# Kernel tuning notes

Hardware: AMD Instinct MI355X
Metric: run time of the kernel (lower is better)

The kernel has to match this reference:

```python
import jax, jax.numpy as jnp
import numpy as np

NEG = -1e10  # matches the -10000000000.0 boundary padding in the torch code


def nw_forward(theta, A):
    """Needleman-Wunsch forward DP with softmax (logsumexp) operator.

    theta: (B, N, M) match potentials; A: (B,) gap penalty.
    Returns Vt: (B,) terminal alignment scores.
    Recursion: V[i,j] = theta[i-1,j-1] + logsumexp(A+V[i-1,j], V[i-1,j-1], A+V[i,j-1]).
    Implemented as scan over rows (i) with an inner scan over columns (j),
    which honors the sequential DP dependencies without Python loops.
    """
    B, N, M = theta.shape
    dtype = theta.dtype
    # V[0, :] row: V[0,0]=0, V[0,j]=NEG for j>=1
    row0 = jnp.full((B, M + 1), NEG, dtype).at[:, 0].set(0.0)

    def row_step(prev_row, th_row):
        # prev_row: (B, M+1) = V[i-1, 0..M]; th_row: (B, M) = theta[:, i-1, :]
        v_up = prev_row[:, 1:]     # V[i-1, j],   j = 1..M
        v_diag = prev_row[:, :-1]  # V[i-1, j-1], j = 1..M

        def col_step(v_left, inp):
            th_j, vu, vd = inp  # each (B,)
            # order (x, m, y) = (A+up, diag, A+left), matching torch stack(v1,v2,v3)
            v = jnp.stack([A + vu, vd, A + v_left], axis=-1)  # (B, 3)
            v_new = th_j + jax.nn.logsumexp(v, axis=-1)
            return v_new, v_new

        xs = (th_row.T, v_up.T, v_diag.T)  # leading axis M
        v_init = jnp.full((B,), NEG, dtype)  # V[i, 0]
        _, row_vals = jax.lax.scan(col_step, v_init, xs)  # (M, B)
        new_row = jnp.concatenate(
            [jnp.full((B, 1), NEG, dtype), row_vals.T], axis=1)  # (B, M+1)
        return new_row, None

    last_row, _ = jax.lax.scan(row_step, row0, jnp.moveaxis(theta, 1, 0))
    return last_row[:, M]  # Vt = V[:, N, M]


def setup_inputs() -> dict:
    key = jax.random.key(0)
    k1, k2 = jax.random.split(key)
    B, N, M = 32, 512, 512
    theta = jax.random.normal(k1, (B, N, M), dtype=jnp.float32)
    A = jax.random.normal(k2, (B,), dtype=jnp.float32)
    return {"theta": theta, "A": A}


def reference(theta, A):
    return nw_forward(theta, A)
```

## Files before the change

### kernel.cpp

```cpp
#include <hip/hip_runtime.h>
#include <math.h>

#define NEGV  -10000000000.0f
#define LOG2E 1.44269504088896340736f
#define LN2F  0.69314718055994530942f

typedef float f4 __attribute__((ext_vector_type(4)));

constexpr int CS    = 16;
constexpr int ROWS  = 80;
constexpr int WL    = 17;
constexpr int CHW   = ROWS * WL;
constexpr int KCMAX = 64;

__global__ __launch_bounds__(512, 2) void nw_kernel(
    const float* __restrict__ theta, const float* __restrict__ A,
    float* __restrict__ out, int N, int M)
{
    __shared__ float thS[8 * 2 * CHW];
    __shared__ float bndD[9 * KCMAX * 16];
    __shared__ int   flg[9 * KCMAX];

    const int tid = threadIdx.x;
    const int w   = tid >> 6;
    const int l   = tid & 63;
    const int j   = tid;
    const int b   = blockIdx.x;
    const int NW  = blockDim.x >> 6;

    for (int i = tid; i < 9 * KCMAX; i += blockDim.x) flg[i] = 0;
    __syncthreads();

    const float a2 = A[b] * LOG2E;
    const float* __restrict__ thb = theta + (size_t)b * N * M;
    const int NM = N * M;

    const int T  = N + M - 1;
    const int KC = (T + CS - 1) / CS;
    const int wstart = 64 * w;
    const int wend   = 64 * w + 63 + N - 1;
    const int ca = wstart / CS;
    const int cb = min(KC - 1, wend / CS);

    const int srow = l >> 4;
    const int sq   = l & 15;
    const int lanebase = srow * (M - 1) + 64 * w + 63 + sq;
    const int wrbase0 = (w * 2 + 0) * CHW + srow * WL + sq;
    const int wrbase1 = (w * 2 + 1) * CHW + srow * WL + sq;
    const int rdbase0 = (w * 2 + 0) * CHW + (63 - l) * WL;
    const int rdbase1 = (w * 2 + 1) * CHW + (63 - l) * WL;

    auto stage_load = [&](int cn, float* stg) {
        const int rb = CS * cn - 64 * w - 63;
        if (rb >= 0 && rb + (ROWS - 1) <= N - 1) {
            const float* p = thb + (size_t)rb * M;
            #pragma unroll
            for (int it = 0; it < 20; ++it) { stg[it] = p[lanebase]; p += 4 * (M - 1); }
        } else {
            const int rbM = rb * M;
            #pragma unroll
            for (int it = 0; it < 20; ++it) {
                int off = rbM + lanebase + it * 4 * (M - 1);
                off = min(max(off, 0), NM - 1);
                stg[it] = thb[off];
            }
        }
    };
    auto stage_write = [&](int cn, const float* stg) {
        const int wb = (cn & 1) ? wrbase1 : wrbase0;
        #pragma unroll
        for (int it = 0; it < 20; ++it) thS[wb + it * 4 * WL] = stg[it] * LOG2E;
    };
    auto wait_flag = [&](int idx) {
        if (__atomic_load_n(&flg[idx], __ATOMIC_ACQUIRE) == 0) {
            do { __builtin_amdgcn_s_sleep(1); }
            while (__atomic_load_n(&flg[idx], __ATOMIC_ACQUIRE) == 0);
        }
    };

    float v_prev = NEGV;
    float v_diag = (j == 0) ? 0.0f : NEGV;
    float bcarry = NEGV;

    {
        float s0[20];
        stage_load(ca, s0);
        stage_write(ca, s0);
        __asm__ volatile("s_waitcnt lgkmcnt(0)" ::: "memory");
    }
    if (w > 0) {
        wait_flag(w * KCMAX + (ca - 1));
        bcarry = bndD[(w * KCMAX + ca - 1) * 16 + 15];
    }

    float stg[20];
    bool have = (ca + 1 <= cb);
    if (have) stage_load(ca + 1, stg);

    for (int c = ca; c <= cb; ++c) {
        const int rdb = (c & 1) ? rdbase1 : rdbase0;
        float th[16];
        #pragma unroll
        for (int k = 0; k < 16; ++k) th[k] = thS[rdb + k * (WL + 1)];

        const bool need_bv = (w > 0) && (CS * c <= 64 * w + N - 1);
        float bv[16];
        if (need_bv) {
            wait_flag(w * KCMAX + c);
            const f4* src = (const f4*)&bndD[(w * KCMAX + c) * 16];
            f4 q0 = src[0], q1 = src[1], q2 = src[2], q3 = src[3];
            bv[0]=q0.x; bv[1]=q0.y; bv[2]=q0.z; bv[3]=q0.w;
            bv[4]=q1.x; bv[5]=q1.y; bv[6]=q1.z; bv[7]=q1.w;
            bv[8]=q2.x; bv[9]=q2.y; bv[10]=q2.z; bv[11]=q2.w;
            bv[12]=q3.x; bv[13]=q3.y; bv[14]=q3.z; bv[15]=q3.w;
        } else {
            #pragma unroll
            for (int k = 0; k < 16; ++k) bv[k] = NEGV;
        }

        float res[16];
        const bool full = (CS * c >= 64 * w + 63) &&
                          (CS * c + CS - 1 <= 64 * w + N - 1);
        if (full) {
            #pragma unroll
            for (int k = 0; k < 16; ++k) {
                float bk = (k == 0) ? bcarry : bv[k - 1];
                float vl = __int_as_float(__builtin_amdgcn_update_dpp(
                    __float_as_int(bk), __float_as_int(v_prev),
                    0x138 , 0xF, 0xF, false));
                float x = a2 + v_prev;
                float z = a2 + vl;
                float m = fmaxf(fmaxf(x, v_diag), z);
                float s = __builtin_amdgcn_exp2f(x - m)
                        + __builtin_amdgcn_exp2f(v_diag - m)
                        + __builtin_amdgcn_exp2f(z - m);
                float v = th[k] + m + __builtin_amdgcn_logf(s);
                res[k] = v;
                v_diag = vl;
                v_prev = v;
            }
        } else {
            const int tmj = CS * c - j;
            #pragma unroll
            for (int k = 0; k < 16; ++k) {
                float bk = (k == 0) ? bcarry : bv[k - 1];
                float vl = __int_as_float(__builtin_amdgcn_update_dpp(
                    __float_as_int(bk), __float_as_int(v_prev),
                    0x138, 0xF, 0xF, false));
                float x = a2 + v_prev;
                float z = a2 + vl;
                float m = fmaxf(fmaxf(x, v_diag), z);
                float s = __builtin_amdgcn_exp2f(x - m)
                        + __builtin_amdgcn_exp2f(v_diag - m)
                        + __builtin_amdgcn_exp2f(z - m);
                float v = th[k] + m + __builtin_amdgcn_logf(s);
                int dt = tmj + k;
                float vn = ((unsigned)dt < (unsigned)N) ? v
                                                        : (dt < 0 ? NEGV : v_prev);
                res[k] = vn;
                v_diag = vl;
                v_prev = vn;
            }
        }

        if (w < NW - 1 && l == 63) {
            f4* dst = (f4*)&bndD[((w + 1) * KCMAX + c) * 16];
            dst[0] = (f4){res[0],  res[1],  res[2],  res[3]};
            dst[1] = (f4){res[4],  res[5],  res[6],  res[7]};
            dst[2] = (f4){res[8],  res[9],  res[10], res[11]};
            dst[3] = (f4){res[12], res[13], res[14], res[15]};
            __atomic_store_n(&flg[(w + 1) * KCMAX + c], 1, __ATOMIC_RELEASE);
        }
        bcarry = bv[15];

        if (have) stage_write(c + 1, stg);
        have = (c + 2 <= cb);
        if (have) stage_load(c + 2, stg);
        __asm__ volatile("s_waitcnt lgkmcnt(0)" ::: "memory");
    }

    if (j == M - 1) out[b] = v_prev * LN2F;
}

extern "C" void kernel_launch(void* const* d_in, const int* in_sizes, int n_in,
                              void* d_out, int out_size, void* d_ws, size_t ws_size,
                              hipStream_t stream) {
    const float* theta = (const float*)d_in[0];
    const float* A     = (const float*)d_in[1];
    float* out = (float*)d_out;

    const int B  = in_sizes[1];
    const int NM = in_sizes[0] / B;
    int N = 1;
    while (N * N < NM) N <<= 1;
    const int M = NM / N;

    hipLaunchKernelGGL(nw_kernel, dim3(B), dim3(M), 0, stream,
                       theta, A, out, N, M);
}
```

Baseline: 182.2 us.

## Split each batch DP across two workgroups linked by global-memory boundary handoff

Each batch element now runs on two 256-thread workgroups, each holding four waves, instead of one 512-thread workgroup. The boundary column between the halves travels through the workspace in global memory, guarded by a magic-value flag, and the next chunk's boundary and flag are prefetched. The goal is to give each wave its own SIMD and reduce contention on the serial wavefront chain. The cost is cross-CU handoff latency, and the design depends on both workgroups being resident at once. The flags are never cleared between calls, so a later launch could read stale values. Local waits also drop the s_sleep backoff.

```diff
diff --git a/kernel.cpp b/kernel.cpp
--- a/kernel.cpp
+++ b/kernel.cpp
@@ -1,9 +1,10 @@
 #include <hip/hip_runtime.h>
 #include <math.h>
 
-#define NEGV  -10000000000.0f
-#define LOG2E 1.44269504088896340736f
-#define LN2F  0.69314718055994530942f
+#define NEGV   -10000000000.0f
+#define LOG2E  1.44269504088896340736f
+#define LN2F   0.69314718055994530942f
+#define MAGICF 0x5CA1AB1Eu
 
 typedef float f4 __attribute__((ext_vector_type(4)));
 
@@ -13,22 +14,24 @@
 constexpr int CHW   = ROWS * WL;
 constexpr int KCMAX = 64;
 
-__global__ __launch_bounds__(512, 2) void nw_kernel(
+__global__ __launch_bounds__(256, 1) void nw_kernel(
     const float* __restrict__ theta, const float* __restrict__ A,
-    float* __restrict__ out, int N, int M)
+    float* __restrict__ out, unsigned* __restrict__ gbnd,
+    unsigned* __restrict__ gflg, int N, int M)
 {
-    __shared__ float thS[8 * 2 * CHW];
-    __shared__ float bndD[9 * KCMAX * 16];
-    __shared__ int   flg[9 * KCMAX];
+    __shared__ float thS[4 * 2 * CHW];
+    __shared__ float bndL[4 * KCMAX * 16];
+    __shared__ int   flgL[4 * KCMAX];
 
     const int tid = threadIdx.x;
-    const int w   = tid >> 6;
+    const int wl  = tid >> 6;
     const int l   = tid & 63;
-    const int j   = tid;
-    const int b   = blockIdx.x;
-    const int NW  = blockDim.x >> 6;
-
-    for (int i = tid; i < 9 * KCMAX; i += blockDim.x) flg[i] = 0;
+    const int h   = blockIdx.x & 1;
+    const int b   = blockIdx.x >> 1;
+    const int wg  = 4 * h + wl;
+    const int j   = 64 * wg + l;
+
+    for (int i = tid; i < 4 * KCMAX; i += blockDim.x) flgL[i] = 0;
     __syncthreads();
 
     const float a2 = A[b] * LOG2E;
@@ -37,21 +40,24 @@
 
     const int T  = N + M - 1;
     const int KC = (T + CS - 1) / CS;
-    const int wstart = 64 * w;
-    const int wend   = 64 * w + 63 + N - 1;
-    const int ca = wstart / CS;
+    const int wend = 64 * wg + 63 + N - 1;
+    const int ca = (64 * wg) / CS;
     const int cb = min(KC - 1, wend / CS);
 
-    const int srow = l >> 4;
-    const int sq   = l & 15;
-    const int lanebase = srow * (M - 1) + 64 * w + 63 + sq;
-    const int wrbase0 = (w * 2 + 0) * CHW + srow * WL + sq;
-    const int wrbase1 = (w * 2 + 1) * CHW + srow * WL + sq;
-    const int rdbase0 = (w * 2 + 0) * CHW + (63 - l) * WL;
-    const int rdbase1 = (w * 2 + 1) * CHW + (63 - l) * WL;
+    const int srow = l >> 4, sq = l & 15;
+    const int lanebase = srow * (M - 1) + 64 * wg + 63 + sq;
+    const int wrbase0 = (wl * 2 + 0) * CHW + srow * WL + sq;
+    const int wrbase1 = (wl * 2 + 1) * CHW + srow * WL + sq;
+    const int rdbase0 = (wl * 2 + 0) * CHW + (63 - l) * WL;
+    const int rdbase1 = (wl * 2 + 1) * CHW + (63 - l) * WL;
+
+    unsigned* gB = gbnd + (size_t)b * KCMAX * 16;
+    unsigned* gF = gflg + b * KCMAX;
+    const bool gsrc = (h == 1) && (wl == 0);
+    const bool gpub = (h == 0) && (wl == 3);
 
     auto stage_load = [&](int cn, float* stg) {
-        const int rb = CS * cn - 64 * w - 63;
+        const int rb = CS * cn - 64 * wg - 63;
         if (rb >= 0 && rb + (ROWS - 1) <= N - 1) {
             const float* p = thb + (size_t)rb * M;
             #pragma unroll
@@ -71,12 +77,6 @@
         #pragma unroll
         for (int it = 0; it < 20; ++it) thS[wb + it * 4 * WL] = stg[it] * LOG2E;
     };
-    auto wait_flag = [&](int idx) {
-        if (__atomic_load_n(&flg[idx], __ATOMIC_ACQUIRE) == 0) {
-            do { __builtin_amdgcn_s_sleep(1); }
-            while (__atomic_load_n(&flg[idx], __ATOMIC_ACQUIRE) == 0);
-        }
-    };
 
     float v_prev = NEGV;
     float v_diag = (j == 0) ? 0.0f : NEGV;
@@ -88,14 +88,25 @@
         stage_write(ca, s0);
         __asm__ volatile("s_waitcnt lgkmcnt(0)" ::: "memory");
     }
-    if (w > 0) {
-        wait_flag(w * KCMAX + (ca - 1));
-        bcarry = bndD[(w * KCMAX + ca - 1) * 16 + 15];
+    if (wl > 0) {
+        const int idx = wl * KCMAX + (ca - 1);
+        while (__atomic_load_n(&flgL[idx], __ATOMIC_ACQUIRE) == 0) {}
+        bcarry = bndL[idx * 16 + 15];
+    } else if (gsrc) {
+        while (__hip_atomic_load(&gF[ca - 1], __ATOMIC_RELAXED,
+                                 __HIP_MEMORY_SCOPE_AGENT) != MAGICF)
+            __builtin_amdgcn_s_sleep(1);
+        bcarry = __uint_as_float(__hip_atomic_load(&gB[(ca - 1) * 16 + 15],
+                    __ATOMIC_RELAXED, __HIP_MEMORY_SCOPE_AGENT));
     }
 
     float stg[20];
     bool have = (ca + 1 <= cb);
     if (have) stage_load(ca + 1, stg);
+
+    unsigned gd[16];
+    unsigned fnext = 0;
+    bool gd_ok = false, fnext_valid = false;
 
     for (int c = ca; c <= cb; ++c) {
         const int rdb = (c & 1) ? rdbase1 : rdbase0;
@@ -103,24 +114,51 @@
         #pragma unroll
         for (int k = 0; k < 16; ++k) th[k] = thS[rdb + k * (WL + 1)];
 
-        const bool need_bv = (w > 0) && (CS * c <= 64 * w + N - 1);
+        const bool need_bv = (wg > 0) && (CS * c <= 64 * wg + N - 1);
         float bv[16];
         if (need_bv) {
-            wait_flag(w * KCMAX + c);
-            const f4* src = (const f4*)&bndD[(w * KCMAX + c) * 16];
-            f4 q0 = src[0], q1 = src[1], q2 = src[2], q3 = src[3];
-            bv[0]=q0.x; bv[1]=q0.y; bv[2]=q0.z; bv[3]=q0.w;
-            bv[4]=q1.x; bv[5]=q1.y; bv[6]=q1.z; bv[7]=q1.w;
-            bv[8]=q2.x; bv[9]=q2.y; bv[10]=q2.z; bv[11]=q2.w;
-            bv[12]=q3.x; bv[13]=q3.y; bv[14]=q3.z; bv[15]=q3.w;
+            if (!gsrc) {
+                const int idx = wl * KCMAX + c;
+                while (__atomic_load_n(&flgL[idx], __ATOMIC_ACQUIRE) == 0) {}
+                const f4* src = (const f4*)&bndL[idx * 16];
+                f4 q0 = src[0], q1 = src[1], q2 = src[2], q3 = src[3];
+                bv[0]=q0.x; bv[1]=q0.y; bv[2]=q0.z; bv[3]=q0.w;
+                bv[4]=q1.x; bv[5]=q1.y; bv[6]=q1.z; bv[7]=q1.w;
+                bv[8]=q2.x; bv[9]=q2.y; bv[10]=q2.z; bv[11]=q2.w;
+                bv[12]=q3.x; bv[13]=q3.y; bv[14]=q3.z; bv[15]=q3.w;
+            } else {
+                if (!gd_ok) {
+                    while (__hip_atomic_load(&gF[c], __ATOMIC_RELAXED,
+                                             __HIP_MEMORY_SCOPE_AGENT) != MAGICF)
+                        __builtin_amdgcn_s_sleep(1);
+                    #pragma unroll
+                    for (int k = 0; k < 16; ++k)
+                        gd[k] = __hip_atomic_load(&gB[c * 16 + k],
+                                    __ATOMIC_RELAXED, __HIP_MEMORY_SCOPE_AGENT);
+                }
+                #pragma unroll
+                for (int k = 0; k < 16; ++k) bv[k] = __uint_as_float(gd[k]);
+                gd_ok = false;
+                if (fnext_valid && fnext == MAGICF) {
+                    #pragma unroll
+                    for (int k = 0; k < 16; ++k)
+                        gd[k] = __hip_atomic_load(&gB[(c + 1) * 16 + k],
+                                    __ATOMIC_RELAXED, __HIP_MEMORY_SCOPE_AGENT);
+                    gd_ok = true;
+                }
+                fnext_valid = (c + 2 <= cb);
+                if (fnext_valid)
+                    fnext = __hip_atomic_load(&gF[c + 2], __ATOMIC_RELAXED,
+                                              __HIP_MEMORY_SCOPE_AGENT);
+            }
         } else {
             #pragma unroll
             for (int k = 0; k < 16; ++k) bv[k] = NEGV;
         }
 
         float res[16];
-        const bool full = (CS * c >= 64 * w + 63) &&
-                          (CS * c + CS - 1 <= 64 * w + N - 1);
+        const bool full = (CS * c >= 64 * wg + 63) &&
+                          (CS * c + CS - 1 <= 64 * wg + N - 1);
         if (full) {
             #pragma unroll
             for (int k = 0; k < 16; ++k) {
@@ -163,17 +201,30 @@
             }
         }
 
-        if (w < NW - 1 && l == 63) {
-            f4* dst = (f4*)&bndD[((w + 1) * KCMAX + c) * 16];
+        if (gpub) {
+            if (l == 63) {
+                #pragma unroll
+                for (int k = 0; k < 16; ++k)
+                    __hip_atomic_store(&gB[c * 16 + k], __float_as_uint(res[k]),
+                                       __ATOMIC_RELAXED, __HIP_MEMORY_SCOPE_AGENT);
+            }
+        } else if (wl < 3 && l == 63) {
+            f4* dst = (f4*)&bndL[((wl + 1) * KCMAX + c) * 16];
             dst[0] = (f4){res[0],  res[1],  res[2],  res[3]};
             dst[1] = (f4){res[4],  res[5],  res[6],  res[7]};
             dst[2] = (f4){res[8],  res[9],  res[10], res[11]};
             dst[3] = (f4){res[12], res[13], res[14], res[15]};
-            __atomic_store_n(&flg[(w + 1) * KCMAX + c], 1, __ATOMIC_RELEASE);
+            __atomic_store_n(&flgL[(wl + 1) * KCMAX + c], 1, __ATOMIC_RELEASE);
         }
         bcarry = bv[15];
 
         if (have) stage_write(c + 1, stg);
+        if (gpub) {
+            __asm__ volatile("s_waitcnt vmcnt(0)" ::: "memory");
+            if (l == 63)
+                __hip_atomic_store(&gF[c], MAGICF,
+                                   __ATOMIC_RELAXED, __HIP_MEMORY_SCOPE_AGENT);
+        }
         have = (c + 2 <= cb);
         if (have) stage_load(c + 2, stg);
         __asm__ volatile("s_waitcnt lgkmcnt(0)" ::: "memory");
@@ -195,6 +246,9 @@
     while (N * N < NM) N <<= 1;
     const int M = NM / N;
 
-    hipLaunchKernelGGL(nw_kernel, dim3(B), dim3(M), 0, stream,
-                       theta, A, out, N, M);
+    unsigned* gbnd = (unsigned*)d_ws;
+    unsigned* gflg = gbnd + (size_t)B * KCMAX * 16;
+
+    hipLaunchKernelGGL(nw_kernel, dim3(B * 2), dim3(M / 2), 0, stream,
+                       theta, A, out, gbnd, gflg, N, M);
 }
```

After: 222.0 us. +21.9%, slower.

## Replace flag handoff with sentinel-polled per-4-column boundary slots between wavefronts

Applied to the files above, without the earlier changes.

Drops the separate flag array and acquire/release atomics. Inter-wavefront boundary values now go through shared-memory slots preset to a sentinel bit pattern, and the consumer spins until every value differs from the sentinel. Handoff granularity shrinks from 16 columns to groups of 4, so the next wavefront can start sooner, and the next slot is prefetched. It also removes the full/partial fast path and the explicit lgkmcnt waits, and lowers launch bounds to one block per unit. This risks correctness, since it relies on ordering of volatile LDS accesses, and the sentinel could collide with a real value.

```diff
diff --git a/kernel.cpp b/kernel.cpp
--- a/kernel.cpp
+++ b/kernel.cpp
@@ -1,25 +1,25 @@
 #include <hip/hip_runtime.h>
 #include <math.h>
 
-#define NEGV  -10000000000.0f
-#define LOG2E 1.44269504088896340736f
-#define LN2F  0.69314718055994530942f
+#define NEGV   -10000000000.0f
+#define LOG2E  1.44269504088896340736f
+#define LN2F   0.69314718055994530942f
+#define SENT   0xAAAAAAAAu
 
 typedef float f4 __attribute__((ext_vector_type(4)));
 
-constexpr int CS    = 16;
-constexpr int ROWS  = 80;
-constexpr int WL    = 17;
-constexpr int CHW   = ROWS * WL;
-constexpr int KCMAX = 64;
+constexpr int CS   = 16;
+constexpr int ROWS = 80;
+constexpr int WL   = 17;
+constexpr int CHW  = ROWS * WL;
+constexpr int GMAX = 256;
 
-__global__ __launch_bounds__(512, 2) void nw_kernel(
+__global__ __launch_bounds__(512, 1) void nw_kernel(
     const float* __restrict__ theta, const float* __restrict__ A,
     float* __restrict__ out, int N, int M)
 {
     __shared__ float thS[8 * 2 * CHW];
-    __shared__ float bndD[9 * KCMAX * 16];
-    __shared__ int   flg[9 * KCMAX];
+    __shared__ f4    bndS[8 * GMAX];
 
     const int tid = threadIdx.x;
     const int w   = tid >> 6;
@@ -28,7 +28,11 @@
     const int b   = blockIdx.x;
     const int NW  = blockDim.x >> 6;
 
-    for (int i = tid; i < 9 * KCMAX; i += blockDim.x) flg[i] = 0;
+    {
+        const float sf = __uint_as_float(SENT);
+        const f4 sv = {sf, sf, sf, sf};
+        for (int i = tid; i < 8 * GMAX; i += blockDim.x) bndS[i] = sv;
+    }
     __syncthreads();
 
     const float a2 = A[b] * LOG2E;
@@ -37,13 +41,12 @@
 
     const int T  = N + M - 1;
     const int KC = (T + CS - 1) / CS;
-    const int wstart = 64 * w;
-    const int wend   = 64 * w + 63 + N - 1;
-    const int ca = wstart / CS;
+    const int wend = 64 * w + 63 + N - 1;
+    const int ca = (64 * w) / CS;
     const int cb = min(KC - 1, wend / CS);
+    const int gmaxw = (64 * w + N - 2) >> 2;
 
-    const int srow = l >> 4;
-    const int sq   = l & 15;
+    const int srow = l >> 4, sq = l & 15;
     const int lanebase = srow * (M - 1) + 64 * w + 63 + sq;
     const int wrbase0 = (w * 2 + 0) * CHW + srow * WL + sq;
     const int wrbase1 = (w * 2 + 1) * CHW + srow * WL + sq;
@@ -71,11 +74,19 @@
         #pragma unroll
         for (int it = 0; it < 20; ++it) thS[wb + it * 4 * WL] = stg[it] * LOG2E;
     };
-    auto wait_flag = [&](int idx) {
-        if (__atomic_load_n(&flg[idx], __ATOMIC_ACQUIRE) == 0) {
-            do { __builtin_amdgcn_s_sleep(1); }
-            while (__atomic_load_n(&flg[idx], __ATOMIC_ACQUIRE) == 0);
-        }
+
+    volatile float* bndV = (volatile float*)bndS;
+    auto bnd_load = [&](int slot) -> f4 {
+        f4 r;
+        r.x = bndV[slot * 4 + 0];
+        r.y = bndV[slot * 4 + 1];
+        r.z = bndV[slot * 4 + 2];
+        r.w = bndV[slot * 4 + 3];
+        return r;
+    };
+    auto bad = [&](f4 v) -> bool {
+        return ((__float_as_uint(v.x) == SENT) | (__float_as_uint(v.y) == SENT) |
+                (__float_as_uint(v.z) == SENT) | (__float_as_uint(v.w) == SENT)) != 0;
     };
 
     float v_prev = NEGV;
@@ -86,12 +97,17 @@
         float s0[20];
         stage_load(ca, s0);
         stage_write(ca, s0);
-        __asm__ volatile("s_waitcnt lgkmcnt(0)" ::: "memory");
+        __asm__ volatile("" ::: "memory");
     }
     if (w > 0) {
-        wait_flag(w * KCMAX + (ca - 1));
-        bcarry = bndD[(w * KCMAX + ca - 1) * 16 + 15];
+        float u;
+        do { u = bndV[(w * GMAX + 16 * w - 1) * 4 + 3]; }
+        while (__float_as_uint(u) == SENT);
+        bcarry = u;
     }
+    f4 nxt;
+    { const float sf = __uint_as_float(SENT); nxt = (f4){sf, sf, sf, sf}; }
+    if (w > 0 && 16 * w <= gmaxw) nxt = bnd_load(w * GMAX + 16 * w);
 
     float stg[20];
     bool have = (ca + 1 <= cb);
@@ -103,50 +119,29 @@
         #pragma unroll
         for (int k = 0; k < 16; ++k) th[k] = thS[rdb + k * (WL + 1)];
 
-        const bool need_bv = (w > 0) && (CS * c <= 64 * w + N - 1);
-        float bv[16];
-        if (need_bv) {
-            wait_flag(w * KCMAX + c);
-            const f4* src = (const f4*)&bndD[(w * KCMAX + c) * 16];
-            f4 q0 = src[0], q1 = src[1], q2 = src[2], q3 = src[3];
-            bv[0]=q0.x; bv[1]=q0.y; bv[2]=q0.z; bv[3]=q0.w;
-            bv[4]=q1.x; bv[5]=q1.y; bv[6]=q1.z; bv[7]=q1.w;
-            bv[8]=q2.x; bv[9]=q2.y; bv[10]=q2.z; bv[11]=q2.w;
-            bv[12]=q3.x; bv[13]=q3.y; bv[14]=q3.z; bv[15]=q3.w;
-        } else {
+        const int tmj = CS * c - j;
+
+        #pragma unroll
+        for (int g = 0; g < 4; ++g) {
+            const int gi = 4 * c + g;
+            float bv0, bv1, bv2, bv3;
+            if (w > 0 && gi <= gmaxw) {
+                f4 cur = nxt;
+                while (bad(cur)) cur = bnd_load(w * GMAX + gi);
+                bv0 = cur.x; bv1 = cur.y; bv2 = cur.z; bv3 = cur.w;
+                if (gi + 1 <= gmaxw) nxt = bnd_load(w * GMAX + gi + 1);
+            } else {
+                bv0 = bv1 = bv2 = bv3 = NEGV;
+            }
+
+            const float bks[4] = {bcarry, bv0, bv1, bv2};
+            float r[4];
             #pragma unroll
-            for (int k = 0; k < 16; ++k) bv[k] = NEGV;
-        }
-
-        float res[16];
-        const bool full = (CS * c >= 64 * w + 63) &&
-                          (CS * c + CS - 1 <= 64 * w + N - 1);
-        if (full) {
-            #pragma unroll
-            for (int k = 0; k < 16; ++k) {
-                float bk = (k == 0) ? bcarry : bv[k - 1];
+            for (int kk = 0; kk < 4; ++kk) {
+                const int k = 4 * g + kk;
                 float vl = __int_as_float(__builtin_amdgcn_update_dpp(
-                    __float_as_int(bk), __float_as_int(v_prev),
+                    __float_as_int(bks[kk]), __float_as_int(v_prev),
                     0x138 , 0xF, 0xF, false));
-                float x = a2 + v_prev;
-                float z = a2 + vl;
-                float m = fmaxf(fmaxf(x, v_diag), z);
-                float s = __builtin_amdgcn_exp2f(x - m)
-                        + __builtin_amdgcn_exp2f(v_diag - m)
-                        + __builtin_amdgcn_exp2f(z - m);
-                float v = th[k] + m + __builtin_amdgcn_logf(s);
-                res[k] = v;
-                v_diag = vl;
-                v_prev = v;
-            }
-        } else {
-            const int tmj = CS * c - j;
-            #pragma unroll
-            for (int k = 0; k < 16; ++k) {
-                float bk = (k == 0) ? bcarry : bv[k - 1];
-                float vl = __int_as_float(__builtin_amdgcn_update_dpp(
-                    __float_as_int(bk), __float_as_int(v_prev),
-                    0x138, 0xF, 0xF, false));
                 float x = a2 + v_prev;
                 float z = a2 + vl;
                 float m = fmaxf(fmaxf(x, v_diag), z);
@@ -157,26 +152,21 @@
                 int dt = tmj + k;
                 float vn = ((unsigned)dt < (unsigned)N) ? v
                                                         : (dt < 0 ? NEGV : v_prev);
-                res[k] = vn;
+                r[kk]  = vn;
                 v_diag = vl;
                 v_prev = vn;
             }
+            bcarry = bv3;
+
+            if (w < NW - 1 && l == 63)
+                bndS[(w + 1) * GMAX + gi] = (f4){r[0], r[1], r[2], r[3]};
+            __asm__ volatile("" ::: "memory");
         }
-
-        if (w < NW - 1 && l == 63) {
-            f4* dst = (f4*)&bndD[((w + 1) * KCMAX + c) * 16];
-            dst[0] = (f4){res[0],  res[1],  res[2],  res[3]};
-            dst[1] = (f4){res[4],  res[5],  res[6],  res[7]};
-            dst[2] = (f4){res[8],  res[9],  res[10], res[11]};
-            dst[3] = (f4){res[12], res[13], res[14], res[15]};
-            __atomic_store_n(&flg[(w + 1) * KCMAX + c], 1, __ATOMIC_RELEASE);
-        }
-        bcarry = bv[15];
 
         if (have) stage_write(c + 1, stg);
         have = (c + 2 <= cb);
         if (have) stage_load(c + 2, stg);
-        __asm__ volatile("s_waitcnt lgkmcnt(0)" ::: "memory");
+        __asm__ volatile("" ::: "memory");
     }
 
     if (j == M - 1) out[b] = v_prev * LN2F;
```

Measured after the change: 243.0 us. +33.4%, slower.
